# Optimization experiments

Measured on AMD Instinct MI355X. Metric: run time of the kernel, lower is better.

## Reference

```python
import jax, jax.numpy as jnp
import numpy as np

N = 50000          # nodes
E = 1_600_000      # edges (avg degree 32)
F_IN = 256
F_OUT = 256
ALPHA = 0.2        # LeakyReLU negative slope


def setup_inputs() -> dict:
    key = jax.random.key(0)
    ks = jax.random.split(key, 7)
    x = jax.random.normal(ks[0], (N, F_IN), dtype=jnp.float32)
    row = jax.random.randint(ks[1], (E,), 0, N, dtype=jnp.int32)  # dst i
    col = jax.random.randint(ks[2], (E,), 0, N, dtype=jnp.int32)  # src j
    W_w = jax.random.normal(ks[3], (F_IN, F_OUT), dtype=jnp.float32) / np.sqrt(F_IN).astype(np.float32)
    W_b = jax.random.normal(ks[4], (F_OUT,), dtype=jnp.float32) * 0.01
    a_w = jax.random.normal(ks[5], (2 * F_OUT,), dtype=jnp.float32) / np.sqrt(2 * F_OUT).astype(np.float32)
    a_b = jax.random.normal(ks[6], (1,), dtype=jnp.float32) * 0.01
    return {"x": x, "W_w": W_w, "W_b": W_b, "a_w": a_w, "a_b": a_b,
            "row": row, "col": col}


def reference(x, W_w, W_b, a_w, a_b, row, col):
    # Wh = W(x): [N, F_OUT]
    Wh = x @ W_w + W_b
    # e[i,j] = leakyrelu(a1 . Wh[j] + a2 . Wh[i] + b)
    # (repeat puts Wh[j] in the first half of the concat, repeat_interleave Wh[i] in the second)
    f_dst_part = Wh @ a_w[:F_OUT]   # contribution of column node j
    f_row_part = Wh @ a_w[F_OUT:]   # contribution of row node i
    e = f_dst_part[col] + f_row_part[row] + a_b[0]          # [E]
    e = jnp.where(e > 0, e, ALPHA * e)                      # LeakyReLU
    # sparse softmax over dim=1 (segment = row i), adjacency values are 1.0
    m = jax.ops.segment_max(e, row, num_segments=N)         # [N]
    ex = jnp.exp(e - m[row])
    denom = jax.ops.segment_sum(ex, row, num_segments=N)    # [N]
    att = ex / denom[row]                                   # [E]
    # h'[i] = sum_j att[i,j] * Wh[j]  (spmm), empty rows stay zero
    h_prime = jax.ops.segment_sum(att[:, None] * Wh[col], row, num_segments=N)
    return jax.nn.relu(h_prime)
```

## Files before the change

kernel.cpp:

```cpp
#include <hip/hip_runtime.h>
#include <math.h>

#define N_NODES 50000
#define N_EDGES 1600000
#define F 256
#define ALPHA 0.2f
#define NP 50048
#define NB 196
#define CAP 10240
#define EPB 4096
#define NAB ((N_EDGES + EPB - 1) / EPB)
#define UNROLL 16
#define GEMM_BLOCKS 782
#define FVEC_BLOCKS ((N_NODES + 3) / 4)

typedef short bf16x8 __attribute__((ext_vector_type(8)));
typedef float f32x4 __attribute__((ext_vector_type(4)));
typedef _Float16 half4 __attribute__((ext_vector_type(4)));

__device__ __forceinline__ unsigned short f2bf(float f) {
  union { float f; unsigned u; } v; v.f = f;
  unsigned u = v.u;
  return (unsigned short)((u + 0x7fffu + ((u >> 16) & 1u)) >> 16);
}

__device__ __forceinline__ unsigned short f2h_bits(float f) {
  union { _Float16 h; unsigned short u; } v;
  v.h = (_Float16)f;
  return v.u;
}

__device__ __forceinline__ float h_bits2f(unsigned short u) {
  union { _Float16 h; unsigned short u; } v;
  v.u = u;
  return (float)v.h;
}

__global__ __launch_bounds__(256) void prep_w(const float* __restrict__ W,
                                              const float* __restrict__ a_w,
                                              const float* __restrict__ W_b,
                                              const float* __restrict__ a_b,
                                              unsigned short* __restrict__ Wt,
                                              float* __restrict__ wa,
                                              float* __restrict__ cb,
                                              int* __restrict__ gcur) {
  if (blockIdx.x == 64) {
    if (threadIdx.x < NB) gcur[threadIdx.x] = 0;
    return;
  }
  const int lane = threadIdx.x & 63, w = threadIdx.x >> 6;
  const int k = blockIdx.x * 4 + w;
  float4 wv = *(const float4*)(W + (size_t)k * F + lane * 4);
  float4 a1 = *(const float4*)(a_w + lane * 4);
  float4 a2 = *(const float4*)(a_w + F + lane * 4);
  Wt[(size_t)(lane * 4 + 0) * F + k] = f2bf(wv.x);
  Wt[(size_t)(lane * 4 + 1) * F + k] = f2bf(wv.y);
  Wt[(size_t)(lane * 4 + 2) * F + k] = f2bf(wv.z);
  Wt[(size_t)(lane * 4 + 3) * F + k] = f2bf(wv.w);
  float s1 = wv.x * a1.x + wv.y * a1.y + wv.z * a1.z + wv.w * a1.w;
  float s2 = wv.x * a2.x + wv.y * a2.y + wv.z * a2.z + wv.w * a2.w;
#pragma unroll
  for (int off = 32; off > 0; off >>= 1) {
    s1 += __shfl_down(s1, off, 64);
    s2 += __shfl_down(s2, off, 64);
  }
  if (lane == 0) { wa[k] = s1; wa[F + k] = s2; }
  if (blockIdx.x == 0 && w == 0) {
    float4 b = *(const float4*)(W_b + lane * 4);
    float t1 = b.x * (a1.x + a2.x) + b.y * (a1.y + a2.y) +
               b.z * (a1.z + a2.z) + b.w * (a1.w + a2.w);
#pragma unroll
    for (int off = 32; off > 0; off >>= 1) t1 += __shfl_down(t1, off, 64);
    if (lane == 0) cb[0] = t1 + a_b[0];
  }
}

#define LDSK 72
__global__ __launch_bounds__(256) void gemm_fvec_binA2(
    const float* __restrict__ x,
    const unsigned short* __restrict__ Wt,
    const float* __restrict__ bias,
    const float* __restrict__ wa,
    const int* __restrict__ row,
    const int* __restrict__ col,
    _Float16* __restrict__ Wh,
    float* __restrict__ f_dst,
    float* __restrict__ f_row,
    int* __restrict__ gcur,
    unsigned* __restrict__ gstage) {
  __shared__ char smem[2 * 128 * LDSK * 2];
  if (blockIdx.x < GEMM_BLOCKS) {
    short* As = (short*)smem;
    short* Bs = As + 128 * LDSK;
    const int tid = threadIdx.x;
    const int lane = tid & 63;
    const int w = tid >> 6;
    const int wm = w >> 1, wn = w & 1;
    const int m0 = (blockIdx.x >> 1) * 128;
    const int n0 = (blockIdx.x & 1) * 128;
    f32x4 acc[4][4] = {{{0.f, 0.f, 0.f, 0.f}}};
    const int srow = tid >> 3;
    const int schunk = tid & 7;
    for (int k0 = 0; k0 < F; k0 += 64) {
#pragma unroll
      for (int i = 0; i < 4; ++i) {
        int r = i * 32 + srow;
        int gm = m0 + r; if (gm > N_NODES - 1) gm = N_NODES - 1;
        const float* src = x + (size_t)gm * F + k0 + schunk * 8;
        float4 lo = *(const float4*)src;
        float4 hi = *(const float4*)(src + 4);
        bf16x8 v;
        v[0] = (short)f2bf(lo.x); v[1] = (short)f2bf(lo.y);
        v[2] = (short)f2bf(lo.z); v[3] = (short)f2bf(lo.w);
        v[4] = (short)f2bf(hi.x); v[5] = (short)f2bf(hi.y);
        v[6] = (short)f2bf(hi.z); v[7] = (short)f2bf(hi.w);
        *(bf16x8*)&As[r * LDSK + schunk * 8] = v;
        *(bf16x8*)&Bs[r * LDSK + schunk * 8] =
            *(const bf16x8*)(Wt + (size_t)(n0 + r) * F + k0 + schunk * 8);
      }
      __syncthreads();
#pragma unroll
      for (int kk = 0; kk < 64; kk += 32) {
        const int rowsel = lane & 15;
        const int ksel = kk + (lane >> 4) * 8;
        bf16x8 af[4], bfr[4];
#pragma unroll
        for (int t = 0; t < 4; ++t) {
          af[t] = *(bf16x8*)&As[(wm * 64 + t * 16 + rowsel) * LDSK + ksel];
          bfr[t] = *(bf16x8*)&Bs[(wn * 64 + t * 16 + rowsel) * LDSK + ksel];
        }
#pragma unroll
        for (int mi = 0; mi < 4; ++mi)
#pragma unroll
          for (int nj = 0; nj < 4; ++nj)
            acc[mi][nj] = __builtin_amdgcn_mfma_f32_16x16x32_bf16(
                af[mi], bfr[nj], acc[mi][nj], 0, 0, 0);
      }
      __syncthreads();
    }
    const int crow = (lane >> 4) * 4;
    const int ccol = lane & 15;
#pragma unroll
    for (int nj = 0; nj < 4; ++nj) {
      int gc = n0 + wn * 64 + nj * 16 + ccol;
      float bv = bias[gc];
#pragma unroll
      for (int mi = 0; mi < 4; ++mi) {
        int gr = m0 + wm * 64 + mi * 16 + crow;
#pragma unroll
        for (int r = 0; r < 4; ++r)
          Wh[(size_t)(gr + r) * F + gc] = (_Float16)(acc[mi][nj][r] + bv);
      }
    }
    return;
  }
  if (blockIdx.x < GEMM_BLOCKS + NAB) {
    int* h = (int*)smem;
    int* lofs = h + NB;
    int* lcur = lofs + NB;
    int* gb = lcur + NB;
    unsigned* stage = (unsigned*)(gb + NB);
    const int t = threadIdx.x;
    for (int i = t; i < NB; i += 256) { h[i] = 0; lcur[i] = 0; }
    __syncthreads();
    const int base = (blockIdx.x - GEMM_BLOCKS) * EPB;
    const int cnt = min(EPB, N_EDGES - base);
#pragma unroll
    for (int j = 0; j < 16; ++j) {
      int k = base + j * 256 + t;
      if (k < N_EDGES) atomicAdd(&h[row[k] >> 8], 1);
    }
    __syncthreads();
    if (t == 0) {
      int run = 0;
      for (int i = 0; i < NB; ++i) { lofs[i] = run; run += h[i]; }
    }
    __syncthreads();
    if (t < NB && h[t] > 0) gb[t] = atomicAdd(&gcur[t], h[t]);
    __syncthreads();
#pragma unroll
    for (int j = 0; j < 16; ++j) {
      int k = base + j * 256 + t;
      if (k < N_EDGES) {
        int r = row[k], b = r >> 8;
        int lp = lofs[b] + atomicAdd(&lcur[b], 1);
        stage[lp] = ((unsigned)b << 24) | ((unsigned)(r & 255) << 16) |
                    (unsigned)col[k];
      }
    }
    __syncthreads();
#pragma unroll
    for (int j = 0; j < 16; ++j) {
      int s = j * 256 + t;
      if (s < cnt) {
        unsigned wv = stage[s];
        int b = wv >> 24;
        gstage[(size_t)b * CAP + gb[b] + (s - lofs[b])] = wv & 0x00FFFFFFu;
      }
    }
    return;
  }
  const int lane = threadIdx.x & 63, w = threadIdx.x >> 6;
  const int node = (blockIdx.x - GEMM_BLOCKS - NAB) * 4 + w;
  if (node >= N_NODES) return;
  float4 xv = *(const float4*)(x + (size_t)node * F + lane * 4);
  float4 v1 = *(const float4*)(wa + lane * 4);
  float4 v2 = *(const float4*)(wa + F + lane * 4);
  float s1 = xv.x * v1.x + xv.y * v1.y + xv.z * v1.z + xv.w * v1.w;
  float s2 = xv.x * v2.x + xv.y * v2.y + xv.z * v2.z + xv.w * v2.w;
#pragma unroll
  for (int off = 32; off > 0; off >>= 1) {
    s1 += __shfl_down(s1, off, 64);
    s2 += __shfl_down(s2, off, 64);
  }
  if (lane == 0) { f_dst[node] = s1; f_row[node] = s2; }
}

__global__ __launch_bounds__(512) void binB(const int* __restrict__ gcur,
                                            const unsigned* __restrict__ gstage,
                                            const float* __restrict__ f_dst,
                                            const float* __restrict__ f_row,
                                            const float* __restrict__ cb,
                                            int2* __restrict__ rsc,
                                            float* __restrict__ inv_denom,
                                            unsigned* __restrict__ csr) {
  __shared__ int cnt[256], cur[256];
  __shared__ float dsum[256];
  const int t = threadIdx.x;
  const int b = blockIdx.x;
  if (t < 256) { cnt[t] = 0; dsum[t] = 0.f; }
  __syncthreads();
  const int nb = gcur[b];
  const int start = b * CAP;
  const float cbs = cb[0];
  for (int s = t; s < nb; s += 512) {
    unsigned wv = gstage[start + s];
    atomicAdd(&cnt[(wv >> 16) & 255], 1);
  }
  __syncthreads();
  if (t == 0) {
    int run = 0;
    for (int i = 0; i < 256; ++i) { int v = cnt[i]; cur[i] = run; run += v; }
  }
  __syncthreads();
  if (t < 256) {
    int g = (b << 8) + t;
    if (g < N_NODES) rsc[g] = make_int2(start + cur[t], cnt[t]);
  }
  __syncthreads();
  for (int s = t; s < nb; s += 512) {
    unsigned wv = gstage[start + s];
    int lr = (wv >> 16) & 255;
    int c = wv & 0xFFFF;
    float ev = f_dst[c] + f_row[(b << 8) + lr] + cbs;
    ev = ev > 0.f ? ev : ALPHA * ev;
    float ex = __expf(ev);
    int p = start + atomicAdd(&cur[lr], 1);
    csr[p] = ((unsigned)f2h_bits(ex) << 16) | (unsigned)c;
    atomicAdd(&dsum[lr], ex);
  }
  __syncthreads();
  if (t < 256) {
    int g = (b << 8) + t;
    if (g < N_NODES) inv_denom[g] = (cnt[t] > 0) ? (1.0f / dsum[t]) : 0.f;
  }
}

__global__ __launch_bounds__(256) void gat_pull(const int2* __restrict__ rsc,
                                                const unsigned* __restrict__ csr,
                                                const float* __restrict__ inv_denom,
                                                const _Float16* __restrict__ Wh,
                                                float* __restrict__ out) {
  const int lane = threadIdx.x & 63, w = threadIdx.x >> 6;
  const int i = blockIdx.x * 4 + w;
  if (i >= N_NODES) return;
  const int2 rc = rsc[i];
  const int s = rc.x, e = rc.x + rc.y;
  const char* whb = (const char*)Wh;
  const unsigned laneoff = (unsigned)lane * 8u;
  float4 acc = make_float4(0.f, 0.f, 0.f, 0.f);
  for (int p = s; p < e; p += UNROLL) {
    unsigned wv[UNROLL];
#pragma unroll
    for (int j = 0; j < UNROLL; ++j) {
      int q = p + j;
      wv[j] = csr[q < e ? q : s];
    }
    half4 v[UNROLL];
#pragma unroll
    for (int j = 0; j < UNROLL; ++j) {
      unsigned off = (wv[j] & 0xFFFFu) * 512u + laneoff;
      v[j] = *(const half4*)(whb + off);
    }
#pragma unroll
    for (int j = 0; j < UNROLL; ++j) {
      float xw = h_bits2f((unsigned short)(wv[j] >> 16));
      xw = (p + j < e) ? xw : 0.f;
      acc.x += xw * (float)v[j][0];
      acc.y += xw * (float)v[j][1];
      acc.z += xw * (float)v[j][2];
      acc.w += xw * (float)v[j][3];
    }
  }
  const float inv = inv_denom[i];
  acc.x = fmaxf(acc.x * inv, 0.f); acc.y = fmaxf(acc.y * inv, 0.f);
  acc.z = fmaxf(acc.z * inv, 0.f); acc.w = fmaxf(acc.w * inv, 0.f);
  ((float4*)out)[(size_t)i * 64 + lane] = acc;
}

extern "C" void kernel_launch(void* const* d_in, const int* in_sizes, int n_in,
                              void* d_out, int out_size, void* d_ws, size_t ws_size,
                              hipStream_t stream) {
  const float* x   = (const float*)d_in[0];
  const float* W_w = (const float*)d_in[1];
  const float* W_b = (const float*)d_in[2];
  const float* a_w = (const float*)d_in[3];
  const float* a_b = (const float*)d_in[4];
  const int*   row = (const int*)d_in[5];
  const int*   col = (const int*)d_in[6];
  float* out = (float*)d_out;

  float* ws = (float*)d_ws;
  size_t off = 0;
  _Float16* Wh = (_Float16*)(ws + off); off += (size_t)NP * F / 2;
  unsigned short* Wt = (unsigned short*)(ws + off); off += (F * F) / 2;
  float* wa = ws + off;            off += 2 * F;
  float* cb = ws + off;            off += 8;
  float* f_dst = ws + off;         off += NP;
  float* f_row = ws + off;         off += NP;
  int* gcur = (int*)(ws + off);    off += NB;
  int2* rsc = (int2*)(ws + off);   off += 2 * (size_t)NP;
  float* inv_denom = (float*)(ws + off); off += NP;
  unsigned* gstage = (unsigned*)(ws + off); off += (size_t)NB * CAP;
  unsigned* csr = (unsigned*)(ws + off); off += (size_t)NB * CAP;
  (void)ws_size; (void)in_sizes; (void)n_in; (void)out_size;

  hipLaunchKernelGGL(prep_w, dim3(65), dim3(256), 0, stream, W_w, a_w, W_b,
                     a_b, Wt, wa, cb, gcur);
  hipLaunchKernelGGL(gemm_fvec_binA2, dim3(GEMM_BLOCKS + NAB + FVEC_BLOCKS),
                     dim3(256), 0, stream, x, Wt, W_b, wa, row, col, Wh,
                     f_dst, f_row, gcur, gstage);
  hipLaunchKernelGGL(binB, dim3(NB), dim3(512), 0, stream, gcur, gstage,
                     f_dst, f_row, cb, rsc, inv_denom, csr);
  hipLaunchKernelGGL(gat_pull, dim3((N_NODES + 3) / 4), dim3(256), 0, stream,
                     rsc, csr, inv_denom, Wh, out);
}
```

Before: 289.2 us.

## Sort CSR edges by source-column bucket within each row and grid-stride fvec blocks

In binB, each row's edges are counted and scattered per (row, column>>13) sub-bucket, so the CSR within a row is roughly ordered by source node. This should give the gather in gat_pull better locality in Wh. Separately, the fvec part of the fused kernel now uses a fixed 2048 blocks that loop over nodes, instead of one block per 4 nodes. The cost is more shared-memory counters, an 8-way prefix per row, and fewer parallel fvec blocks.

```diff
diff --git a/kernel.cpp b/kernel.cpp
--- a/kernel.cpp
+++ b/kernel.cpp
@@ -12,7 +12,7 @@
 #define NAB ((N_EDGES + EPB - 1) / EPB)
 #define UNROLL 16
 #define GEMM_BLOCKS 782
-#define FVEC_BLOCKS ((N_NODES + 3) / 4)
+#define FVEC_SLOTS 2048
 
 typedef short bf16x8 __attribute__((ext_vector_type(8)));
 typedef float f32x4 __attribute__((ext_vector_type(4)));
@@ -201,19 +201,20 @@
     return;
   }
   const int lane = threadIdx.x & 63, w = threadIdx.x >> 6;
-  const int node = (blockIdx.x - GEMM_BLOCKS - NAB) * 4 + w;
-  if (node >= N_NODES) return;
-  float4 xv = *(const float4*)(x + (size_t)node * F + lane * 4);
+  const int slot = blockIdx.x - GEMM_BLOCKS - NAB;
   float4 v1 = *(const float4*)(wa + lane * 4);
   float4 v2 = *(const float4*)(wa + F + lane * 4);
-  float s1 = xv.x * v1.x + xv.y * v1.y + xv.z * v1.z + xv.w * v1.w;
-  float s2 = xv.x * v2.x + xv.y * v2.y + xv.z * v2.z + xv.w * v2.w;
-#pragma unroll
-  for (int off = 32; off > 0; off >>= 1) {
-    s1 += __shfl_down(s1, off, 64);
-    s2 += __shfl_down(s2, off, 64);
-  }
-  if (lane == 0) { f_dst[node] = s1; f_row[node] = s2; }
+  for (int node = slot * 4 + w; node < N_NODES; node += FVEC_SLOTS * 4) {
+    float4 xv = *(const float4*)(x + (size_t)node * F + lane * 4);
+    float s1 = xv.x * v1.x + xv.y * v1.y + xv.z * v1.z + xv.w * v1.w;
+    float s2 = xv.x * v2.x + xv.y * v2.y + xv.z * v2.z + xv.w * v2.w;
+#pragma unroll
+    for (int off = 32; off > 0; off >>= 1) {
+      s1 += __shfl_down(s1, off, 64);
+      s2 += __shfl_down(s2, off, 64);
+    }
+    if (lane == 0) { f_dst[node] = s1; f_row[node] = s2; }
+  }
 }
 
 __global__ __launch_bounds__(512) void binB(const int* __restrict__ gcur,
@@ -224,28 +225,43 @@
                                             int2* __restrict__ rsc,
                                             float* __restrict__ inv_denom,
                                             unsigned* __restrict__ csr) {
-  __shared__ int cnt[256], cur[256];
+  __shared__ int cnt2[2048];
+  __shared__ int cur2[2048];
+  __shared__ int rcnt[256], rbase[256];
   __shared__ float dsum[256];
   const int t = threadIdx.x;
   const int b = blockIdx.x;
-  if (t < 256) { cnt[t] = 0; dsum[t] = 0.f; }
+  for (int i = t; i < 2048; i += 512) cnt2[i] = 0;
+  if (t < 256) dsum[t] = 0.f;
   __syncthreads();
   const int nb = gcur[b];
   const int start = b * CAP;
   const float cbs = cb[0];
   for (int s = t; s < nb; s += 512) {
     unsigned wv = gstage[start + s];
-    atomicAdd(&cnt[(wv >> 16) & 255], 1);
+    int key = (((wv >> 16) & 255) << 3) | ((wv & 0xFFFFu) >> 13);
+    atomicAdd(&cnt2[key], 1);
+  }
+  __syncthreads();
+  if (t < 256) {
+    int tot = 0;
+#pragma unroll
+    for (int q = 0; q < 8; ++q) tot += cnt2[t * 8 + q];
+    rcnt[t] = tot;
   }
   __syncthreads();
   if (t == 0) {
     int run = 0;
-    for (int i = 0; i < 256; ++i) { int v = cnt[i]; cur[i] = run; run += v; }
+    for (int i = 0; i < 256; ++i) { rbase[i] = run; run += rcnt[i]; }
   }
   __syncthreads();
   if (t < 256) {
+    int base = start + rbase[t];
     int g = (b << 8) + t;
-    if (g < N_NODES) rsc[g] = make_int2(start + cur[t], cnt[t]);
+    if (g < N_NODES) rsc[g] = make_int2(base, rcnt[t]);
+    int run = base;
+#pragma unroll
+    for (int q = 0; q < 8; ++q) { cur2[t * 8 + q] = run; run += cnt2[t * 8 + q]; }
   }
   __syncthreads();
   for (int s = t; s < nb; s += 512) {
@@ -255,14 +271,14 @@
     float ev = f_dst[c] + f_row[(b << 8) + lr] + cbs;
     ev = ev > 0.f ? ev : ALPHA * ev;
     float ex = __expf(ev);
-    int p = start + atomicAdd(&cur[lr], 1);
+    int p = atomicAdd(&cur2[(lr << 3) | (c >> 13)], 1);
     csr[p] = ((unsigned)f2h_bits(ex) << 16) | (unsigned)c;
     atomicAdd(&dsum[lr], ex);
   }
   __syncthreads();
   if (t < 256) {
     int g = (b << 8) + t;
-    if (g < N_NODES) inv_denom[g] = (cnt[t] > 0) ? (1.0f / dsum[t]) : 0.f;
+    if (g < N_NODES) inv_denom[g] = (rcnt[t] > 0) ? (1.0f / dsum[t]) : 0.f;
   }
 }
 
@@ -337,7 +353,7 @@
 
   hipLaunchKernelGGL(prep_w, dim3(65), dim3(256), 0, stream, W_w, a_w, W_b,
                      a_b, Wt, wa, cb, gcur);
-  hipLaunchKernelGGL(gemm_fvec_binA2, dim3(GEMM_BLOCKS + NAB + FVEC_BLOCKS),
+  hipLaunchKernelGGL(gemm_fvec_binA2, dim3(GEMM_BLOCKS + NAB + FVEC_SLOTS),
                      dim3(256), 0, stream, x, Wt, W_b, wa, row, col, Wh,
                      f_dst, f_row, gcur, gstage);
   hipLaunchKernelGGL(binB, dim3(NB), dim3(512), 0, stream, gcur, gstage,
```

Measured after the change: 281.5 us. -2.7%, faster.
